# Kernel tuning notes

Measured on AMD Instinct MI355X. Metric: run time of the kernel, lower is better.

Reference implementation:

```python
import jax, jax.numpy as jnp
import numpy as np

B, T, C = 1, 4096, 1024
N_HEAD = 16
HEAD_DIM = C // N_HEAD
SCALE = 1.0 / np.sqrt(HEAD_DIM).astype(np.float32)


def setup_inputs() -> dict:
    key = jax.random.key(0)
    k1, k2, k3 = jax.random.split(key, 3)
    x = jax.random.normal(k1, (B, T, C), dtype=jnp.float32)
    W_attn = jax.random.normal(k2, (C, 3 * C), dtype=jnp.float32) * 0.02
    b_attn = jnp.zeros((3 * C,), dtype=jnp.float32)
    W_proj = jax.random.normal(k3, (C, C), dtype=jnp.float32) * 0.02
    b_proj = jnp.zeros((C,), dtype=jnp.float32)
    return {"x": x, "W_attn": W_attn, "b_attn": b_attn, "W_proj": W_proj, "b_proj": b_proj}


def reference(x, W_attn, b_attn, W_proj, b_proj):
    Bq, Tq, Cq = x.shape
    qkv = x @ W_attn + b_attn                      # [B, T, 3C]
    q, k, v = jnp.split(qkv, 3, axis=-1)
    # split heads -> [B, H, T, D]
    def split_heads(t):
        return t.reshape(Bq, Tq, N_HEAD, HEAD_DIM).transpose(0, 2, 1, 3)
    q, k, v = split_heads(q), split_heads(k), split_heads(v)
    scores = jnp.einsum('bhqd,bhkd->bhqk', q, k) * SCALE  # [B, H, T, T]
    causal = jnp.tril(jnp.ones((Tq, Tq), dtype=bool))
    scores = jnp.where(causal[None, None], scores, jnp.float32(-jnp.inf))
    probs = jax.nn.softmax(scores, axis=-1)
    out = jnp.einsum('bhqk,bhkd->bhqd', probs, v)          # [B, H, T, D]
    out = out.transpose(0, 2, 1, 3).reshape(Bq, Tq, Cq)    # merge heads
    out = out @ W_proj + b_proj
    return out
```

## Files before the change

kernel.cpp:

```cpp
#include <hip/hip_runtime.h>
#include <hip/hip_bf16.h>


typedef unsigned short u16;
typedef u16 u16x4 __attribute__((ext_vector_type(4)));
typedef u16 u16x8 __attribute__((ext_vector_type(8)));
typedef __bf16 bf16x8 __attribute__((ext_vector_type(8)));
typedef float f32x4 __attribute__((ext_vector_type(4)));

#define T_SEQ 4096
#define C_DIM 1024
#define NH 16
#define HD 64
#define QSC 0.18033688f
#define NJOBS 2304

static __device__ __forceinline__ u16 f2bf(float f) {
    __hip_bfloat16 h = __float2bfloat16(f);
    return __builtin_bit_cast(u16, h);
}

static __device__ __forceinline__ float bf2f(u16 u) {
    return __builtin_bit_cast(float, (unsigned)u << 16);
}

static __device__ __forceinline__ bf16x8 ldfr(const u16* base, int byteoff) {
    return __builtin_bit_cast(bf16x8, *(const u16x8*)(base + (byteoff >> 1)));
}

static __device__ __forceinline__ void gld_lds16(const void* g, void* l) {
    __builtin_amdgcn_global_load_lds((const __attribute__((address_space(1))) void*)g,
                                     (__attribute__((address_space(3))) void*)l, 16, 0, 0);
}

#define MFMA16(a, b, c) __builtin_amdgcn_mfma_f32_16x16x32_bf16((a), (b), (c), 0, 0, 0)


__global__ __launch_bounds__(256) void k_cvt_x(const float* __restrict__ x, u16* __restrict__ xb) {
    int i = (blockIdx.x * 256 + threadIdx.x) * 8;
    float4 a = *(const float4*)(x + i);
    float4 b = *(const float4*)(x + i + 4);
    u16x8 o;
    o[0] = f2bf(a.x); o[1] = f2bf(a.y); o[2] = f2bf(a.z); o[3] = f2bf(a.w);
    o[4] = f2bf(b.x); o[5] = f2bf(b.y); o[6] = f2bf(b.z); o[7] = f2bf(b.w);
    *(u16x8*)(xb + i) = o;
}

__global__ __launch_bounds__(256) void k_transpose_w(const float* __restrict__ src,
                                                     u16* __restrict__ dst, int R, int Cc) {
    __shared__ float tile[32][33];
    int bx = blockIdx.x * 32;
    int by = blockIdx.y * 32;
    int x = threadIdx.x, y = threadIdx.y;
#pragma unroll
    for (int i = 0; i < 32; i += 8)
        tile[y + i][x] = src[(by + y + i) * Cc + bx + x];
    __syncthreads();
#pragma unroll
    for (int i = 0; i < 32; i += 8)
        dst[(bx + y + i) * R + by + x] = f2bf(tile[x][y + i]);
}


template <int EPI>
__global__ __launch_bounds__(256) void k_gemm(const u16* __restrict__ A, const u16* __restrict__ Bt,
                                              const float* __restrict__ bias,
                                              u16* __restrict__ outQ, u16* __restrict__ outK,
                                              u16* __restrict__ outVt, float* __restrict__ outF,
                                              int kd, int nbx) {
    __shared__ u16 Al[128 * 64];
    __shared__ u16 Bl[128 * 64];
    const int tid = threadIdx.x;
    const int lane = tid & 63;
    const int wid = tid >> 6;
    const int wm = wid >> 1, wn = wid & 1;
    const int c = lane & 15, g = lane >> 4;
    const int nwg = gridDim.x;
    const int swzb = ((int)blockIdx.x & 7) * (nwg >> 3) + ((int)blockIdx.x >> 3);
    const int m0 = (swzb % nbx) * 128;
    const int n0 = (swzb / nbx) * 128;
    const int srow = lane >> 3;
    const int sxu = (((lane & 7) * 16) ^ (srow << 4)) >> 1;
    const int swa = (c & 7) << 4;

    f32x4 acc[4][4] = {};

    for (int k0 = 0; k0 < kd; k0 += 64) {
#pragma unroll
        for (int i = 0; i < 4; ++i) {
            const int ch = wid * 4 + i;
            const int row = ch * 8 + srow;
            gld_lds16(A + (m0 + row) * kd + k0 + sxu, &Al[ch * 512]);
            gld_lds16(Bt + (n0 + row) * kd + k0 + sxu, &Bl[ch * 512]);
        }
        __syncthreads();
        bf16x8 af[4][2], bfm[4][2];
#pragma unroll
        for (int mi = 0; mi < 4; ++mi) {
            const u16* p = Al + (wm * 64 + mi * 16 + c) * 64;
            af[mi][0] = ldfr(p, (16 * g) ^ swa);
            af[mi][1] = ldfr(p, (64 + 16 * g) ^ swa);
        }
#pragma unroll
        for (int ni = 0; ni < 4; ++ni) {
            const u16* p = Bl + (wn * 64 + ni * 16 + c) * 64;
            bfm[ni][0] = ldfr(p, (16 * g) ^ swa);
            bfm[ni][1] = ldfr(p, (64 + 16 * g) ^ swa);
        }
#pragma unroll
        for (int mi = 0; mi < 4; ++mi)
#pragma unroll
            for (int ni = 0; ni < 4; ++ni) {
                acc[mi][ni] = MFMA16(af[mi][0], bfm[ni][0], acc[mi][ni]);
                acc[mi][ni] = MFMA16(af[mi][1], bfm[ni][1], acc[mi][ni]);
            }
        __syncthreads();
    }

    const int mbase = m0 + wm * 64;
    const int nbase = n0 + wn * 64;
    if (EPI == 0) {
        const int part = m0 >> 10;
#pragma unroll
        for (int mi = 0; mi < 4; ++mi) {
            const int fbase = mbase + mi * 16 + 4 * g;
            const f32x4 bv = *(const f32x4*)(bias + fbase);
            const int fr = fbase & 1023;
            const int h = fr >> 6, d0 = fr & 63;
#pragma unroll
            for (int ni = 0; ni < 4; ++ni) {
                const int tok = nbase + ni * 16 + c;
                if (part == 2) {
#pragma unroll
                    for (int r = 0; r < 4; ++r)
                        outVt[(size_t)(fr + r) * T_SEQ + tok] = f2bf(acc[mi][ni][r] + bv[r]);
                } else {
                    u16x4 pk;
#pragma unroll
                    for (int r = 0; r < 4; ++r) {
                        float v = acc[mi][ni][r] + bv[r];
                        pk[r] = f2bf(part == 0 ? v * QSC : v);
                    }
                    u16* dst = (part == 0 ? outQ : outK);
                    *(u16x4*)(dst + (size_t)(h * T_SEQ + tok) * HD + d0) = pk;
                }
            }
        }
    } else {
#pragma unroll
        for (int mi = 0; mi < 4; ++mi) {
            const int fbase = mbase + mi * 16 + 4 * g;
            const f32x4 bv = *(const f32x4*)(bias + fbase);
#pragma unroll
            for (int ni = 0; ni < 4; ++ni) {
                const int tok = nbase + ni * 16 + c;
                f32x4 w;
#pragma unroll
                for (int r = 0; r < 4; ++r) w[r] = acc[mi][ni][r] + bv[r];
                *(f32x4*)(outF + (size_t)tok * C_DIM + fbase) = w;
            }
        }
    }
}


static __device__ __forceinline__ void p_gen(f32x4 s[4], int qabs, int kv0, int g,
                                             bool domask, bf16x8 pa[2]) {
    if (domask) {
#pragma unroll
        for (int tau = 0; tau < 4; ++tau) {
            const int kb = kv0 + 32 * (tau >> 1) + 4 * (tau & 1) + 8 * g;
#pragma unroll
            for (int r = 0; r < 4; ++r)
                if (kb + r > qabs) s[tau][r] = -3e38f;
        }
    }
    u16 pb[4][4];
#pragma unroll
    for (int tau = 0; tau < 4; ++tau)
#pragma unroll
        for (int r = 0; r < 4; ++r)
            pb[tau][r] = f2bf(__builtin_amdgcn_exp2f(s[tau][r]));
    const u16x8 p0 = {pb[0][0], pb[0][1], pb[0][2], pb[0][3], pb[1][0], pb[1][1], pb[1][2], pb[1][3]};
    const u16x8 p1 = {pb[2][0], pb[2][1], pb[2][2], pb[2][3], pb[3][0], pb[3][1], pb[3][2], pb[3][3]};
    pa[0] = __builtin_bit_cast(bf16x8, p0);
    pa[1] = __builtin_bit_cast(bf16x8, p1);
}

__global__ __launch_bounds__(256) void k_flash(const u16* __restrict__ Qg, const u16* __restrict__ Kg,
                                               const u16* __restrict__ Vtg,
                                               u16* __restrict__ part, float* __restrict__ lpart,
                                               unsigned* __restrict__ cnt) {
    __shared__ u16 sm[2][2][4096];
    volatile unsigned* jw = (volatile unsigned*)&sm[0][0][0];

    const int tid = threadIdx.x;
    const int lane = tid & 63;
    const int wid = tid >> 6;
    const int c = lane & 15, g = lane >> 4;
    const int srow = lane >> 3;
    const int sxu = (((lane & 7) * 16) ^ (srow << 4)) >> 1;

    const u16x8 onespat = {0x3F80, 0x3F80, 0x3F80, 0x3F80, 0x3F80, 0x3F80, 0x3F80, 0x3F80};
    const bf16x8 onesf = __builtin_bit_cast(bf16x8, onespat);

    for (;;) {
        if (tid == 0) *jw = atomicAdd(cnt, 1u);
        __syncthreads();
        const unsigned j = *jw;
        __syncthreads();
        if (j >= (unsigned)NJOBS) break;

        const int head = (int)(j & 15u);
        const int idx = (int)(j >> 4);
        int qb, ch, nc;
        if (idx < 32)       { qb = 31 - (idx >> 3); ch = idx & 7; nc = 8; }
        else if (idx < 60)  { const int t = idx - 32;  qb = 27 - t / 7;    ch = t % 7; nc = 7; }
        else if (idx < 84)  { const int t = idx - 60;  qb = 23 - t / 6;    ch = t % 6; nc = 6; }
        else if (idx < 104) { const int t = idx - 84;  qb = 19 - t / 5;    ch = t % 5; nc = 5; }
        else if (idx < 120) { const int t = idx - 104; qb = 15 - (t >> 2); ch = t & 3; nc = 4; }
        else if (idx < 132) { const int t = idx - 120; qb = 11 - t / 3;    ch = t % 3; nc = 3; }
        else if (idx < 140) { const int t = idx - 132; qb = 7 - (t >> 1);  ch = t & 1; nc = 2; }
        else                { qb = 3 - (idx - 140); ch = 0; nc = 1; }
        const int ntile = 2 * qb + 2;
        const int cbase = ntile / nc, crem = ntile % nc;
        const int len = cbase + (ch < crem ? 1 : 0);
        const int start = ch * cbase + (ch < crem ? ch : crem);

        const int q0w = qb * 128 + wid * 32;

        const u16* Qh = Qg + (size_t)head * (T_SEQ * HD);
        const u16* Kh = Kg + (size_t)head * (T_SEQ * HD);
        const u16* Vh = Vtg + (size_t)head * (HD * T_SEQ);

        bf16x8 qf[2][2];
#pragma unroll
        for (int h = 0; h < 2; ++h)
#pragma unroll
            for (int dc = 0; dc < 2; ++dc)
                qf[h][dc] = __builtin_bit_cast(
                    bf16x8, *(const u16x8*)(Qh + (q0w + 16 * h + c) * HD + dc * 32 + 8 * g));

        f32x4 o0[4] = {}, o1[4] = {}, ol0 = {}, ol1 = {};

        {
            const int kvs = start * 64;
#pragma unroll
            for (int i = 0; i < 2; ++i) {
                const int chk = wid * 2 + i;
                gld_lds16(Kh + (kvs + chk * 8 + srow) * HD + sxu, &sm[0][0][chk * 512]);
                gld_lds16(Vh + (chk * 8 + srow) * T_SEQ + kvs + sxu, &sm[0][1][chk * 512]);
            }
        }
        __syncthreads();

        for (int t = 0; t < len; ++t) {
            const int cur = t & 1;
            const int kv0 = (start + t) * 64;
            if (t + 1 < len) {
                const int kvn = kv0 + 64;
#pragma unroll
                for (int i = 0; i < 2; ++i) {
                    const int chk = wid * 2 + i;
                    gld_lds16(Kh + (kvn + chk * 8 + srow) * HD + sxu, &sm[cur ^ 1][0][chk * 512]);
                    gld_lds16(Vh + (chk * 8 + srow) * T_SEQ + kvn + sxu, &sm[cur ^ 1][1][chk * 512]);
                }
            }
            const u16* Kl = &sm[cur][0][0];
            const u16* Vl = &sm[cur][1][0];
            f32x4 s0[4], s1[4];
            __builtin_amdgcn_s_setprio(1);
#pragma unroll
            for (int tau = 0; tau < 4; ++tau) {
                const int prow = 32 * (tau >> 1) + 4 * (tau & 1) + 8 * (c >> 2) + (c & 3);
                const int sw = (prow & 7) << 4;
                const u16* kb = Kl + prow * 64;
                const bf16x8 k0 = ldfr(kb, (16 * g) ^ sw);
                const bf16x8 k1 = ldfr(kb, (64 + 16 * g) ^ sw);
                f32x4 z0 = {}, z1 = {};
                z0 = MFMA16(k0, qf[0][0], z0);
                s0[tau] = MFMA16(k1, qf[0][1], z0);
                z1 = MFMA16(k0, qf[1][0], z1);
                s1[tau] = MFMA16(k1, qf[1][1], z1);
            }
            __builtin_amdgcn_s_setprio(0);
            const bool dm0 = (kv0 + 63) > (q0w);
            const bool dm1 = (kv0 + 63) > (q0w + 16);
            bf16x8 pa0[2], pa1[2];
            p_gen(s0, q0w + c, kv0, g, dm0, pa0);
            p_gen(s1, q0w + 16 + c, kv0, g, dm1, pa1);
            const int swv = (c & 7) << 4;
            __builtin_amdgcn_s_setprio(1);
#pragma unroll
            for (int n = 0; n < 4; ++n) {
                const u16* vb = Vl + (n * 16 + c) * 64;
                const bf16x8 v0 = ldfr(vb, (16 * g) ^ swv);
                const bf16x8 v1 = ldfr(vb, (64 + 16 * g) ^ swv);
                o0[n] = MFMA16(v0, pa0[0], o0[n]);
                o0[n] = MFMA16(v1, pa0[1], o0[n]);
                o1[n] = MFMA16(v0, pa1[0], o1[n]);
                o1[n] = MFMA16(v1, pa1[1], o1[n]);
            }
            ol0 = MFMA16(onesf, pa0[0], ol0);
            ol0 = MFMA16(onesf, pa0[1], ol0);
            ol1 = MFMA16(onesf, pa1[0], ol1);
            ol1 = MFMA16(onesf, pa1[1], ol1);
            __builtin_amdgcn_s_setprio(0);
            __syncthreads();
        }

        u16* slot = part + (size_t)j * 8192u;
        float* lsl = lpart + (size_t)j * 128u;
        const int ql0 = wid * 32 + c;
#pragma unroll
        for (int n = 0; n < 4; ++n) {
            u16x4 w0, w1;
#pragma unroll
            for (int r = 0; r < 4; ++r) {
                w0[r] = f2bf(o0[n][r]);
                w1[r] = f2bf(o1[n][r]);
            }
            *(u16x4*)(slot + ql0 * 64 + n * 16 + 4 * g) = w0;
            *(u16x4*)(slot + (ql0 + 16) * 64 + n * 16 + 4 * g) = w1;
        }
        if (g == 0) {
            lsl[ql0] = ol0[0];
            lsl[ql0 + 16] = ol1[0];
        }
        __syncthreads();
    }
}


__global__ __launch_bounds__(256) void k_combine(const u16* __restrict__ part,
                                                 const float* __restrict__ lpart,
                                                 u16* __restrict__ Ab) {
    const int head = blockIdx.x >> 5, qb = blockIdx.x & 31;
    int nc, idx0;
    if (qb >= 28)      { nc = 8; idx0 = (31 - qb) * 8; }
    else if (qb >= 24) { nc = 7; idx0 = 32 + (27 - qb) * 7; }
    else if (qb >= 20) { nc = 6; idx0 = 60 + (23 - qb) * 6; }
    else if (qb >= 16) { nc = 5; idx0 = 84 + (19 - qb) * 5; }
    else if (qb >= 12) { nc = 4; idx0 = 104 + (15 - qb) * 4; }
    else if (qb >= 8)  { nc = 3; idx0 = 120 + (11 - qb) * 3; }
    else if (qb >= 4)  { nc = 2; idx0 = 132 + (7 - qb) * 2; }
    else               { nc = 1; idx0 = 140 + (3 - qb); }

    const int q = threadIdx.x >> 1;
    const int dh = (threadIdx.x & 1) * 32;
    float acc[32] = {};
    float l = 0.f;
    for (int i = 0; i < nc; ++i) {
        const unsigned jj = (unsigned)(((idx0 + i) << 4) | head);
        const u16* sp = part + (size_t)jj * 8192u + q * 64 + dh;
#pragma unroll
        for (int v = 0; v < 4; ++v) {
            const u16x8 w = *(const u16x8*)(sp + 8 * v);
#pragma unroll
            for (int e = 0; e < 8; ++e) acc[8 * v + e] += bf2f(w[e]);
        }
        l += lpart[(size_t)jj * 128u + q];
    }
    const float li = 1.0f / l;
    u16* dst = Ab + (size_t)(qb * 128 + q) * C_DIM + head * HD + dh;
#pragma unroll
    for (int v = 0; v < 4; ++v) {
        u16x8 w;
#pragma unroll
        for (int e = 0; e < 8; ++e) w[e] = f2bf(acc[8 * v + e] * li);
        *(u16x8*)(dst + 8 * v) = w;
    }
}


extern "C" void kernel_launch(void* const* d_in, const int* in_sizes, int n_in,
                              void* d_out, int out_size, void* d_ws, size_t ws_size,
                              hipStream_t stream) {
    const float* x      = (const float*)d_in[0];
    const float* W_attn = (const float*)d_in[1];
    const float* b_attn = (const float*)d_in[2];
    const float* W_proj = (const float*)d_in[3];
    const float* b_proj = (const float*)d_in[4];
    float* out = (float*)d_out;

    char* ws = (char*)d_ws;
    u16* xb    = (u16*)(ws);
    u16* Wat   = (u16*)(ws + (8u << 20));
    u16* Wpt   = (u16*)(ws + (14u << 20));
    u16* Qb    = (u16*)(ws + (16u << 20));
    u16* Kb    = (u16*)(ws + (24u << 20));
    u16* Vtb   = (u16*)(ws + (32u << 20));
    u16* prt   = (u16*)(ws + (40u << 20));
    float* lpt = (float*)(ws + (78u << 20));
    u16* Ab    = xb;

    unsigned* cnt = (unsigned*)d_out;
    hipMemsetAsync(cnt, 0, 4, stream);

    k_cvt_x<<<2048, 256, 0, stream>>>(x, xb);
    k_transpose_w<<<dim3(96, 32), dim3(32, 8), 0, stream>>>(W_attn, Wat, 1024, 3072);
    k_transpose_w<<<dim3(32, 32), dim3(32, 8), 0, stream>>>(W_proj, Wpt, 1024, 1024);
    k_gemm<0><<<768, 256, 0, stream>>>(Wat, xb, b_attn, Qb, Kb, Vtb, nullptr, 1024, 24);
    k_flash<<<1280, 256, 0, stream>>>(Qb, Kb, Vtb, prt, lpt, cnt);
    k_combine<<<512, 256, 0, stream>>>(prt, lpt, Ab);
    k_gemm<1><<<256, 256, 0, stream>>>(Wpt, Ab, b_proj, nullptr, nullptr, nullptr, out, 1024, 8);
}
```

Baseline: 172.4 us.

## Use 256-row query blocks with 8-wave flash blocks and direct single-chunk output

Result: faster. 165.4 us (median of 2 runs) (-4.1%).

```diff
diff --git a/kernel.cpp b/kernel.cpp
--- a/kernel.cpp
+++ b/kernel.cpp
@@ -13,7 +13,7 @@
 #define NH 16
 #define HD 64
 #define QSC 0.18033688f
-#define NJOBS 2304
+#define NJOBS 1152
 
 static __device__ __forceinline__ u16 f2bf(float f) {
     __hip_bfloat16 h = __float2bfloat16(f);
@@ -187,8 +187,8 @@
     pa[1] = __builtin_bit_cast(bf16x8, p1);
 }
 
-__global__ __launch_bounds__(256) void k_flash(const u16* __restrict__ Qg, const u16* __restrict__ Kg,
-                                               const u16* __restrict__ Vtg,
+__global__ __launch_bounds__(512) void k_flash(const u16* __restrict__ Qg, const u16* __restrict__ Kg,
+                                               const u16* __restrict__ Vtg, u16* __restrict__ Ab,
                                                u16* __restrict__ part, float* __restrict__ lpart,
                                                unsigned* __restrict__ cnt) {
     __shared__ u16 sm[2][2][4096];
@@ -214,20 +214,20 @@
         const int head = (int)(j & 15u);
         const int idx = (int)(j >> 4);
         int qb, ch, nc;
-        if (idx < 32)       { qb = 31 - (idx >> 3); ch = idx & 7; nc = 8; }
-        else if (idx < 60)  { const int t = idx - 32;  qb = 27 - t / 7;    ch = t % 7; nc = 7; }
-        else if (idx < 84)  { const int t = idx - 60;  qb = 23 - t / 6;    ch = t % 6; nc = 6; }
-        else if (idx < 104) { const int t = idx - 84;  qb = 19 - t / 5;    ch = t % 5; nc = 5; }
-        else if (idx < 120) { const int t = idx - 104; qb = 15 - (t >> 2); ch = t & 3; nc = 4; }
-        else if (idx < 132) { const int t = idx - 120; qb = 11 - t / 3;    ch = t % 3; nc = 3; }
-        else if (idx < 140) { const int t = idx - 132; qb = 7 - (t >> 1);  ch = t & 1; nc = 2; }
-        else                { qb = 3 - (idx - 140); ch = 0; nc = 1; }
-        const int ntile = 2 * qb + 2;
+        if (idx < 16)      { qb = 15 - (idx >> 3); ch = idx & 7; nc = 8; }
+        else if (idx < 30) { const int t = idx - 16; qb = 13 - t / 7;    ch = t % 7; nc = 7; }
+        else if (idx < 42) { const int t = idx - 30; qb = 11 - t / 6;    ch = t % 6; nc = 6; }
+        else if (idx < 52) { const int t = idx - 42; qb = 9 - t / 5;     ch = t % 5; nc = 5; }
+        else if (idx < 60) { const int t = idx - 52; qb = 7 - (t >> 2);  ch = t & 3; nc = 4; }
+        else if (idx < 66) { const int t = idx - 60; qb = 5 - t / 3;     ch = t % 3; nc = 3; }
+        else if (idx < 70) { const int t = idx - 66; qb = 3 - (t >> 1);  ch = t & 1; nc = 2; }
+        else               { qb = 1 - (idx - 70); ch = 0; nc = 1; }
+        const int ntile = 4 * qb + 4;
         const int cbase = ntile / nc, crem = ntile % nc;
         const int len = cbase + (ch < crem ? 1 : 0);
         const int start = ch * cbase + (ch < crem ? ch : crem);
 
-        const int q0w = qb * 128 + wid * 32;
+        const int q0w = qb * 256 + wid * 32;
 
         const u16* Qh = Qg + (size_t)head * (T_SEQ * HD);
         const u16* Kh = Kg + (size_t)head * (T_SEQ * HD);
@@ -245,12 +245,8 @@
 
         {
             const int kvs = start * 64;
-#pragma unroll
-            for (int i = 0; i < 2; ++i) {
-                const int chk = wid * 2 + i;
-                gld_lds16(Kh + (kvs + chk * 8 + srow) * HD + sxu, &sm[0][0][chk * 512]);
-                gld_lds16(Vh + (chk * 8 + srow) * T_SEQ + kvs + sxu, &sm[0][1][chk * 512]);
-            }
+            gld_lds16(Kh + (kvs + wid * 8 + srow) * HD + sxu, &sm[0][0][wid * 512]);
+            gld_lds16(Vh + (wid * 8 + srow) * T_SEQ + kvs + sxu, &sm[0][1][wid * 512]);
         }
         __syncthreads();
 
@@ -259,92 +255,107 @@
             const int kv0 = (start + t) * 64;
             if (t + 1 < len) {
                 const int kvn = kv0 + 64;
-#pragma unroll
-                for (int i = 0; i < 2; ++i) {
-                    const int chk = wid * 2 + i;
-                    gld_lds16(Kh + (kvn + chk * 8 + srow) * HD + sxu, &sm[cur ^ 1][0][chk * 512]);
-                    gld_lds16(Vh + (chk * 8 + srow) * T_SEQ + kvn + sxu, &sm[cur ^ 1][1][chk * 512]);
+                gld_lds16(Kh + (kvn + wid * 8 + srow) * HD + sxu, &sm[cur ^ 1][0][wid * 512]);
+                gld_lds16(Vh + (wid * 8 + srow) * T_SEQ + kvn + sxu, &sm[cur ^ 1][1][wid * 512]);
+            }
+            if (kv0 <= q0w + 31) {
+                const u16* Kl = &sm[cur][0][0];
+                const u16* Vl = &sm[cur][1][0];
+                f32x4 s0[4], s1[4];
+                __builtin_amdgcn_s_setprio(1);
+#pragma unroll
+                for (int tau = 0; tau < 4; ++tau) {
+                    const int prow = 32 * (tau >> 1) + 4 * (tau & 1) + 8 * (c >> 2) + (c & 3);
+                    const int sw = (prow & 7) << 4;
+                    const u16* kb = Kl + prow * 64;
+                    const bf16x8 k0 = ldfr(kb, (16 * g) ^ sw);
+                    const bf16x8 k1 = ldfr(kb, (64 + 16 * g) ^ sw);
+                    f32x4 z0 = {}, z1 = {};
+                    z0 = MFMA16(k0, qf[0][0], z0);
+                    s0[tau] = MFMA16(k1, qf[0][1], z0);
+                    z1 = MFMA16(k0, qf[1][0], z1);
+                    s1[tau] = MFMA16(k1, qf[1][1], z1);
                 }
-            }
-            const u16* Kl = &sm[cur][0][0];
-            const u16* Vl = &sm[cur][1][0];
-            f32x4 s0[4], s1[4];
-            __builtin_amdgcn_s_setprio(1);
-#pragma unroll
-            for (int tau = 0; tau < 4; ++tau) {
-                const int prow = 32 * (tau >> 1) + 4 * (tau & 1) + 8 * (c >> 2) + (c & 3);
-                const int sw = (prow & 7) << 4;
-                const u16* kb = Kl + prow * 64;
-                const bf16x8 k0 = ldfr(kb, (16 * g) ^ sw);
-                const bf16x8 k1 = ldfr(kb, (64 + 16 * g) ^ sw);
-                f32x4 z0 = {}, z1 = {};
-                z0 = MFMA16(k0, qf[0][0], z0);
-                s0[tau] = MFMA16(k1, qf[0][1], z0);
-                z1 = MFMA16(k0, qf[1][0], z1);
-                s1[tau] = MFMA16(k1, qf[1][1], z1);
-            }
-            __builtin_amdgcn_s_setprio(0);
-            const bool dm0 = (kv0 + 63) > (q0w);
-            const bool dm1 = (kv0 + 63) > (q0w + 16);
-            bf16x8 pa0[2], pa1[2];
-            p_gen(s0, q0w + c, kv0, g, dm0, pa0);
-            p_gen(s1, q0w + 16 + c, kv0, g, dm1, pa1);
-            const int swv = (c & 7) << 4;
-            __builtin_amdgcn_s_setprio(1);
+                __builtin_amdgcn_s_setprio(0);
+                const bool dm0 = (kv0 + 63) > (q0w);
+                const bool dm1 = (kv0 + 63) > (q0w + 16);
+                bf16x8 pa0[2], pa1[2];
+                p_gen(s0, q0w + c, kv0, g, dm0, pa0);
+                p_gen(s1, q0w + 16 + c, kv0, g, dm1, pa1);
+                const int swv = (c & 7) << 4;
+                __builtin_amdgcn_s_setprio(1);
+#pragma unroll
+                for (int n = 0; n < 4; ++n) {
+                    const u16* vb = Vl + (n * 16 + c) * 64;
+                    const bf16x8 v0 = ldfr(vb, (16 * g) ^ swv);
+                    const bf16x8 v1 = ldfr(vb, (64 + 16 * g) ^ swv);
+                    o0[n] = MFMA16(v0, pa0[0], o0[n]);
+                    o0[n] = MFMA16(v1, pa0[1], o0[n]);
+                    o1[n] = MFMA16(v0, pa1[0], o1[n]);
+                    o1[n] = MFMA16(v1, pa1[1], o1[n]);
+                }
+                ol0 = MFMA16(onesf, pa0[0], ol0);
+                ol0 = MFMA16(onesf, pa0[1], ol0);
+                ol1 = MFMA16(onesf, pa1[0], ol1);
+                ol1 = MFMA16(onesf, pa1[1], ol1);
+                __builtin_amdgcn_s_setprio(0);
+            }
+            __syncthreads();
+        }
+
+        const int ql0 = wid * 32 + c;
+        if (nc == 1) {
+            const float li0 = 1.0f / ol0[0], li1 = 1.0f / ol1[0];
+            u16* dst0 = Ab + (size_t)(qb * 256 + ql0) * C_DIM + head * HD;
+            u16* dst1 = dst0 + (size_t)16 * C_DIM;
 #pragma unroll
             for (int n = 0; n < 4; ++n) {
-                const u16* vb = Vl + (n * 16 + c) * 64;
-                const bf16x8 v0 = ldfr(vb, (16 * g) ^ swv);
-                const bf16x8 v1 = ldfr(vb, (64 + 16 * g) ^ swv);
-                o0[n] = MFMA16(v0, pa0[0], o0[n]);
-                o0[n] = MFMA16(v1, pa0[1], o0[n]);
-                o1[n] = MFMA16(v0, pa1[0], o1[n]);
-                o1[n] = MFMA16(v1, pa1[1], o1[n]);
-            }
-            ol0 = MFMA16(onesf, pa0[0], ol0);
-            ol0 = MFMA16(onesf, pa0[1], ol0);
-            ol1 = MFMA16(onesf, pa1[0], ol1);
-            ol1 = MFMA16(onesf, pa1[1], ol1);
-            __builtin_amdgcn_s_setprio(0);
-            __syncthreads();
-        }
-
-        u16* slot = part + (size_t)j * 8192u;
-        float* lsl = lpart + (size_t)j * 128u;
-        const int ql0 = wid * 32 + c;
-#pragma unroll
-        for (int n = 0; n < 4; ++n) {
-            u16x4 w0, w1;
-#pragma unroll
-            for (int r = 0; r < 4; ++r) {
-                w0[r] = f2bf(o0[n][r]);
-                w1[r] = f2bf(o1[n][r]);
-            }
-            *(u16x4*)(slot + ql0 * 64 + n * 16 + 4 * g) = w0;
-            *(u16x4*)(slot + (ql0 + 16) * 64 + n * 16 + 4 * g) = w1;
-        }
-        if (g == 0) {
-            lsl[ql0] = ol0[0];
-            lsl[ql0 + 16] = ol1[0];
-        }
-        __syncthreads();
-    }
-}
-
-
-__global__ __launch_bounds__(256) void k_combine(const u16* __restrict__ part,
+                u16x4 w0, w1;
+#pragma unroll
+                for (int r = 0; r < 4; ++r) {
+                    w0[r] = f2bf(o0[n][r] * li0);
+                    w1[r] = f2bf(o1[n][r] * li1);
+                }
+                *(u16x4*)(dst0 + n * 16 + 4 * g) = w0;
+                *(u16x4*)(dst1 + n * 16 + 4 * g) = w1;
+            }
+        } else {
+            u16* slot = part + (size_t)j * 16384u;
+            float* lsl = lpart + (size_t)j * 256u;
+#pragma unroll
+            for (int n = 0; n < 4; ++n) {
+                u16x4 w0, w1;
+#pragma unroll
+                for (int r = 0; r < 4; ++r) {
+                    w0[r] = f2bf(o0[n][r]);
+                    w1[r] = f2bf(o1[n][r]);
+                }
+                *(u16x4*)(slot + ql0 * 64 + n * 16 + 4 * g) = w0;
+                *(u16x4*)(slot + (ql0 + 16) * 64 + n * 16 + 4 * g) = w1;
+            }
+            if (g == 0) {
+                lsl[ql0] = ol0[0];
+                lsl[ql0 + 16] = ol1[0];
+            }
+        }
+        __syncthreads();
+    }
+}
+
+
+__global__ __launch_bounds__(512) void k_combine(const u16* __restrict__ part,
                                                  const float* __restrict__ lpart,
                                                  u16* __restrict__ Ab) {
-    const int head = blockIdx.x >> 5, qb = blockIdx.x & 31;
+    const int head = blockIdx.x / 14;
+    const int qb = 2 + (blockIdx.x % 14);
     int nc, idx0;
-    if (qb >= 28)      { nc = 8; idx0 = (31 - qb) * 8; }
-    else if (qb >= 24) { nc = 7; idx0 = 32 + (27 - qb) * 7; }
-    else if (qb >= 20) { nc = 6; idx0 = 60 + (23 - qb) * 6; }
-    else if (qb >= 16) { nc = 5; idx0 = 84 + (19 - qb) * 5; }
-    else if (qb >= 12) { nc = 4; idx0 = 104 + (15 - qb) * 4; }
-    else if (qb >= 8)  { nc = 3; idx0 = 120 + (11 - qb) * 3; }
-    else if (qb >= 4)  { nc = 2; idx0 = 132 + (7 - qb) * 2; }
-    else               { nc = 1; idx0 = 140 + (3 - qb); }
+    if (qb >= 14)      { nc = 8; idx0 = (15 - qb) * 8; }
+    else if (qb >= 12) { nc = 7; idx0 = 16 + (13 - qb) * 7; }
+    else if (qb >= 10) { nc = 6; idx0 = 30 + (11 - qb) * 6; }
+    else if (qb >= 8)  { nc = 5; idx0 = 42 + (9 - qb) * 5; }
+    else if (qb >= 6)  { nc = 4; idx0 = 52 + (7 - qb) * 4; }
+    else if (qb >= 4)  { nc = 3; idx0 = 60 + (5 - qb) * 3; }
+    else               { nc = 2; idx0 = 66 + (3 - qb) * 2; }
 
     const int q = threadIdx.x >> 1;
     const int dh = (threadIdx.x & 1) * 32;
@@ -352,17 +363,17 @@
     float l = 0.f;
     for (int i = 0; i < nc; ++i) {
         const unsigned jj = (unsigned)(((idx0 + i) << 4) | head);
-        const u16* sp = part + (size_t)jj * 8192u + q * 64 + dh;
+        const u16* sp = part + (size_t)jj * 16384u + q * 64 + dh;
 #pragma unroll
         for (int v = 0; v < 4; ++v) {
             const u16x8 w = *(const u16x8*)(sp + 8 * v);
 #pragma unroll
             for (int e = 0; e < 8; ++e) acc[8 * v + e] += bf2f(w[e]);
         }
-        l += lpart[(size_t)jj * 128u + q];
+        l += lpart[(size_t)jj * 256u + q];
     }
     const float li = 1.0f / l;
-    u16* dst = Ab + (size_t)(qb * 128 + q) * C_DIM + head * HD + dh;
+    u16* dst = Ab + (size_t)(qb * 256 + q) * C_DIM + head * HD + dh;
 #pragma unroll
     for (int v = 0; v < 4; ++v) {
         u16x8 w;
@@ -401,7 +412,7 @@
     k_transpose_w<<<dim3(96, 32), dim3(32, 8), 0, stream>>>(W_attn, Wat, 1024, 3072);
     k_transpose_w<<<dim3(32, 32), dim3(32, 8), 0, stream>>>(W_proj, Wpt, 1024, 1024);
     k_gemm<0><<<768, 256, 0, stream>>>(Wat, xb, b_attn, Qb, Kb, Vtb, nullptr, 1024, 24);
-    k_flash<<<1280, 256, 0, stream>>>(Qb, Kb, Vtb, prt, lpt, cnt);
-    k_combine<<<512, 256, 0, stream>>>(prt, lpt, Ab);
+    k_flash<<<512, 512, 0, stream>>>(Qb, Kb, Vtb, Ab, prt, lpt, cnt);
+    k_combine<<<224, 512, 0, stream>>>(prt, lpt, Ab);
     k_gemm<1><<<256, 256, 0, stream>>>(Wpt, Ab, b_proj, nullptr, nullptr, nullptr, out, 1024, 8);
 }
```
